# Kernel tuning notes

Hardware: AMD Instinct MI355X
Metric: run time of the kernel (lower is better)

## Reference

```python
import jax, jax.numpy as jnp
from jax import lax
import numpy as np

N_FFT = 256
HOP = 128
NUM_EXPERTS = 8
TOPK = 2
B = 128
L = 4096


def conv1d(x, w, b, pad):
    # x [N,C,T], w [O,I,K]
    y = lax.conv_general_dilated(x, w, (1,), [(pad, pad)],
                                 dimension_numbers=('NCH', 'OIH', 'NCH'))
    return y + b[None, :, None]


def maxpool1d(x, p):
    return lax.reduce_window(x, -jnp.inf, lax.max, (1, 1, p), (1, 1, p), 'VALID')


def se_block(x, w1, w2):
    # x [B,C,T]; squeeze-excitation with no-bias linears
    y = x.mean(-1)
    y = jax.nn.relu(y @ w1.T)
    y = jax.nn.sigmoid(y @ w2.T)
    return x * y[:, :, None]


def interp_linear(x, out_len):
    # F.interpolate(mode='linear', align_corners=False) on [B,C,T]
    Lin = x.shape[-1]
    scale = Lin / out_len
    coords = jnp.clip((jnp.arange(out_len, dtype=x.dtype) + 0.5) * scale - 0.5, 0.0, Lin - 1)
    lo = jnp.floor(coords).astype(jnp.int32)
    hi = jnp.minimum(lo + 1, Lin - 1)
    w = (coords - lo).astype(x.dtype)
    return x[..., lo] * (1.0 - w) + x[..., hi] * w


def lstm_scan(x, wih, whh, bih, bhh):
    # x [T,B,D] -> hidden seq [T,B,H]; torch gate order i,f,g,o
    H = whh.shape[1]
    def step(carry, xt):
        h, c = carry
        gates = xt @ wih.T + h @ whh.T + bih + bhh
        i, f, g, o = jnp.split(gates, 4, axis=-1)
        c = jax.nn.sigmoid(f) * c + jax.nn.sigmoid(i) * jnp.tanh(g)
        h = jax.nn.sigmoid(o) * jnp.tanh(c)
        return (h, c), h
    z = jnp.zeros((x.shape[1], H), x.dtype)
    _, hs = lax.scan(step, (z, z), x)
    return hs


def _forward(x_continuum, x_normalized,
             gate_w1, gate_b1, gate_w2, gate_b2,
             exp_w1, exp_b1, exp_w2, exp_b2,
             lw1, lb1, lw2, lb2, se2_w1, se2_w2, lw3, lb3, se3_w1, se3_w2,
             wih_f, whh_f, bih_f, bhh_f, wih_b, whh_b, bih_b, bhh_b,
             ffn_w1, ffn_b1, ffn_w2, ffn_b2):
    Bsz = x_continuum.shape[0]
    # --- STFT magnitude (center=True, reflect pad, periodic hann window) ---
    n = jnp.arange(N_FFT, dtype=x_continuum.dtype)
    win = 0.5 * (1.0 - jnp.cos(2.0 * jnp.pi * n / N_FFT))
    xp = jnp.pad(x_continuum, ((0, 0), (N_FFT // 2, N_FFT // 2)), mode='reflect')
    n_frames = 1 + (xp.shape[1] - N_FFT) // HOP  # 33
    idx = jnp.arange(n_frames)[:, None] * HOP + jnp.arange(N_FFT)[None, :]
    frames = xp[:, idx] * win                      # [B,T,N_FFT]
    mag = jnp.abs(jnp.fft.rfft(frames, axis=-1)).transpose(0, 2, 1)  # [B,129,T]
    mag = mag.astype(x_continuum.dtype)
    # --- gating: mean-pool over time, MLP, top-k, softmax over top-k ---
    pooled = mag.mean(-1)                          # [B,129]
    logits = jax.nn.relu(pooled @ gate_w1.T + gate_b1) @ gate_w2.T + gate_b2
    topv, topi = lax.top_k(logits, TOPK)
    gw = jax.nn.softmax(topv, axis=1)              # [B,K]
    # --- dense all-expert conv pyramids (matches original dense compute) ---
    def expert(w1, b1, w2, b2):
        h = jax.nn.relu(conv1d(mag, w1, b1, 2))
        return jax.nn.relu(conv1d(h, w2, b2, 1))
    eo = jax.vmap(expert)(exp_w1, exp_b1, exp_w2, exp_b2)  # [E,B,C,T]
    sel = eo[topi, jnp.arange(Bsz)[:, None]]               # [B,K,C,T]
    freq_feat = jnp.einsum('bk,bkct->bct', gw, sel)        # [B,256,33]
    # --- line attention branch ---
    h = jax.nn.relu(conv1d(x_normalized[:, None, :], lw1, lb1, 3))
    h = maxpool1d(h, 4)
    h = jax.nn.relu(conv1d(h, lw2, lb2, 2))
    h = se_block(h, se2_w1, se2_w2)
    h = maxpool1d(h, 4)
    h = jax.nn.relu(conv1d(h, lw3, lb3, 1))
    h = se_block(h, se3_w1, se3_w2)
    line_feat = maxpool1d(h, 4)                            # [B,256,64]
    # --- length alignment via linear interpolation ---
    t = min(freq_feat.shape[-1], line_feat.shape[-1])
    freq_feat = interp_linear(freq_feat, t)
    line_feat = interp_linear(line_feat, t)
    comb = jnp.concatenate([freq_feat, line_feat], axis=1).transpose(2, 0, 1)  # [T,B,512]
    # --- single-layer bidirectional LSTM, take last time step ---
    hf = lstm_scan(comb, wih_f, whh_f, bih_f, bhh_f)
    hb = lstm_scan(comb[::-1], wih_b, whh_b, bih_b, bhh_b)[::-1]
    last = jnp.concatenate([hf[-1], hb[-1]], axis=-1)      # [B,512]
    # --- prediction head (dropout inactive at inference) ---
    h = jax.nn.relu(last @ ffn_w1.T + ffn_b1)
    return h @ ffn_w2.T + ffn_b2                           # [B,1]


def setup_inputs() -> dict:
    key = jax.random.key(0)
    ks = jax.random.split(key, 40)
    def rn(k, shape, s=0.05):
        return jax.random.normal(k, shape, dtype=jnp.float32) * s
    d = {
        'x_continuum': jax.random.normal(ks[0], (B, L), jnp.float32),
        'x_normalized': jax.random.normal(ks[1], (B, L), jnp.float32),
        'gate_w1': rn(ks[2], (128, 129)), 'gate_b1': rn(ks[3], (128,)),
        'gate_w2': rn(ks[4], (NUM_EXPERTS, 128)), 'gate_b2': rn(ks[5], (NUM_EXPERTS,)),
        'exp_w1': rn(ks[6], (NUM_EXPERTS, 256, 129, 5)), 'exp_b1': rn(ks[7], (NUM_EXPERTS, 256)),
        'exp_w2': rn(ks[8], (NUM_EXPERTS, 256, 256, 3)), 'exp_b2': rn(ks[9], (NUM_EXPERTS, 256)),
        'lw1': rn(ks[10], (64, 1, 7)), 'lb1': rn(ks[11], (64,)),
        'lw2': rn(ks[12], (128, 64, 5)), 'lb2': rn(ks[13], (128,)),
        'se2_w1': rn(ks[14], (32, 128)), 'se2_w2': rn(ks[15], (128, 32)),
        'lw3': rn(ks[16], (256, 128, 3)), 'lb3': rn(ks[17], (256,)),
        'se3_w1': rn(ks[18], (64, 256)), 'se3_w2': rn(ks[19], (256, 64)),
        'wih_f': rn(ks[20], (1024, 512)), 'whh_f': rn(ks[21], (1024, 256)),
        'bih_f': rn(ks[22], (1024,)), 'bhh_f': rn(ks[23], (1024,)),
        'wih_b': rn(ks[24], (1024, 512)), 'whh_b': rn(ks[25], (1024, 256)),
        'bih_b': rn(ks[26], (1024,)), 'bhh_b': rn(ks[27], (1024,)),
        'ffn_w1': rn(ks[28], (256, 512)), 'ffn_b1': rn(ks[29], (256,)),
        'ffn_w2': rn(ks[30], (1, 256)), 'ffn_b2': rn(ks[31], (1,)),
    }
    return d


def reference(x_continuum, x_normalized,
              gate_w1, gate_b1, gate_w2, gate_b2,
              exp_w1, exp_b1, exp_w2, exp_b2,
              lw1, lb1, lw2, lb2, se2_w1, se2_w2, lw3, lb3, se3_w1, se3_w2,
              wih_f, whh_f, bih_f, bhh_f, wih_b, whh_b, bih_b, bhh_b,
              ffn_w1, ffn_b1, ffn_w2, ffn_b2):
    return _forward(x_continuum, x_normalized,
                    gate_w1, gate_b1, gate_w2, gate_b2,
                    exp_w1, exp_b1, exp_w2, exp_b2,
                    lw1, lb1, lw2, lb2, se2_w1, se2_w2, lw3, lb3, se3_w1, se3_w2,
                    wih_f, whh_f, bih_f, bhh_f, wih_b, whh_b, bih_b, bhh_b,
                    ffn_w1, ffn_b1, ffn_w2, ffn_b2)
```

## Files before the change

### kernel.cpp

```cpp
#include <hip/hip_runtime.h>
#include <math.h>

namespace {
constexpr int B = 128;
constexpr int L = 4096;
constexpr int NBIN = 129;
constexpr int NFR = 33;

constexpr size_t F_MAG    = 0;
constexpr size_t F_GW     = F_MAG + 544896;
constexpr size_t F_TOPI   = F_GW + 256;
constexpr size_t F_EH1    = F_TOPI + 256;
constexpr size_t F_SEL    = F_EH1 + 2162688;
constexpr size_t F_LINEF  = F_SEL + 2162688;
constexpr size_t F_COMB   = F_LINEF + 2097152;
constexpr size_t F_XPROJ  = F_COMB + 2162688;
constexpr size_t F_GATESB = F_XPROJ + 4325376;
constexpr size_t F_HF     = F_GATESB + 131072;
constexpr size_t F_HBLAST = F_HF + 32768;
constexpr size_t F_SESUM2 = F_HBLAST + 32768;
constexpr size_t F_SESC2  = F_SESUM2 + 16384;
constexpr size_t F_SESUM3 = F_SESC2 + 16384;
constexpr size_t F_SESC3  = F_SESUM3 + 32768;
constexpr size_t F_WHHB   = F_SESC3 + 32768;
constexpr size_t F_WKB    = F_WHHB + 131072;
constexpr size_t F_WKB3   = F_WKB + 20480;
constexpr size_t F_WIHF   = F_WKB3 + 49152;
constexpr size_t F_WIHB   = F_WIHF + 262144;
constexpr size_t F_BIGA   = F_WIHB + 262144;
constexpr size_t F_BIGB   = F_BIGA + 8388608;
constexpr size_t A_WKBE1  = F_XPROJ;
constexpr size_t A_WKBE2  = F_XPROJ + 720896;
constexpr size_t A_MAGT   = F_XPROJ + 1507328;

constexpr int PB_E1   = 5632;
constexpr int PB_E2   = PB_E1 + 6144;
constexpr int PB_WKB  = PB_E2 + 160;
constexpr int PB_WKB3 = PB_WKB + 384;
constexpr int PB_WF   = PB_WKB3 + 512;
constexpr int PB_WB   = PB_WF + 512;
constexpr int PB_WHH  = PB_WB + 128;
constexpr int PB_Z2   = PB_WHH + 64;
constexpr int PB_Z3   = PB_Z2 + 128;
}

typedef __attribute__((ext_vector_type(8))) short bf16x8;
typedef __attribute__((ext_vector_type(4))) float f32x4;

__device__ __forceinline__ float sigm(float x) { return 1.0f / (1.0f + expf(-x)); }
__device__ __forceinline__ float fsigm(float x) { return 1.0f / (1.0f + __expf(-x)); }
__device__ __forceinline__ float ftanh(float x) { return 1.0f - 2.0f / (__expf(2.0f * x) + 1.0f); }

__device__ __forceinline__ unsigned int f2bf_rne(float f) {
    unsigned int u = __float_as_uint(f);
    return (u + 0x7FFFu + ((u >> 16) & 1u)) >> 16;
}
__device__ __forceinline__ float bflo(unsigned int u) { return __uint_as_float(u << 16); }
__device__ __forceinline__ float bfhi(unsigned int u) { return __uint_as_float(u & 0xFFFF0000u); }
__device__ __forceinline__ float bf2f(unsigned short s) { return __uint_as_float(((unsigned int)s) << 16); }

__global__ __launch_bounds__(256) void prep_all_kernel(const float* __restrict__ exp_w1,
                                                       const float* __restrict__ exp_w2,
                                                       const float* __restrict__ lw2,
                                                       const float* __restrict__ lw3,
                                                       const float* __restrict__ wih_f,
                                                       const float* __restrict__ wih_b,
                                                       const float* __restrict__ whh_f,
                                                       unsigned short* __restrict__ wkbE1,
                                                       unsigned short* __restrict__ wkbE2,
                                                       unsigned short* __restrict__ wkb,
                                                       unsigned short* __restrict__ wkb3,
                                                       unsigned short* __restrict__ wihFb,
                                                       unsigned short* __restrict__ wihBb,
                                                       uint4* __restrict__ whh4,
                                                       float* __restrict__ seSum2,
                                                       float* __restrict__ seSum3)
{
    int bid = blockIdx.x, tid = threadIdx.x;
    if (bid < PB_E1) {
        int idx = bid * 256 + tid;
        int eo = idx / 704, K = idx % 704;
        int k = K / 136, ic = K - k * 136;
        float v = (k < 5 && ic < 129) ? exp_w1[((size_t)eo * 129 + ic) * 5 + k] : 0.f;
        wkbE1[idx] = (unsigned short)f2bf_rne(v);
    } else if (bid < PB_E2) {
        int idx = (bid - PB_E1) * 256 + tid;
        int eo = idx / 768, K = idx % 768;
        int k = K >> 8, ic = K & 255;
        wkbE2[idx] = (unsigned short)f2bf_rne(exp_w2[((size_t)eo * 256 + ic) * 3 + k]);
    } else if (bid < PB_WKB) {
        int idx = (bid - PB_E2) * 256 + tid;
        int oc = idx / 320, K = idx % 320;
        int k = K >> 6, ic = K & 63;
        wkb[idx] = (unsigned short)f2bf_rne(lw2[oc * 320 + ic * 5 + k]);
    } else if (bid < PB_WKB3) {
        int idx = (bid - PB_WKB) * 256 + tid;
        int oc = idx / 384, K = idx % 384;
        int k = K >> 7, ic = K & 127;
        wkb3[idx] = (unsigned short)f2bf_rne(lw3[oc * 384 + ic * 3 + k]);
    } else if (bid < PB_WF) {
        int i = ((bid - PB_WKB3) * 256 + tid) * 4;
        float4 v = *reinterpret_cast<const float4*>(wih_f + i);
        uint2 w;
        w.x = f2bf_rne(v.x) | (f2bf_rne(v.y) << 16);
        w.y = f2bf_rne(v.z) | (f2bf_rne(v.w) << 16);
        *reinterpret_cast<uint2*>(wihFb + i) = w;
    } else if (bid < PB_WB) {
        int i = ((bid - PB_WF) * 256 + tid) * 4;
        float4 v = *reinterpret_cast<const float4*>(wih_b + i);
        uint2 w;
        w.x = f2bf_rne(v.x) | (f2bf_rne(v.y) << 16);
        w.y = f2bf_rne(v.z) | (f2bf_rne(v.w) << 16);
        *reinterpret_cast<uint2*>(wihBb + i) = w;
    } else if (bid < PB_WHH) {
        int idx = (bid - PB_WB) * 256 + tid;
        int k8 = idx >> 10, j = idx & 1023;
        const float* src = whh_f + (size_t)j * 256 + k8 * 8;
        float4 v0 = *reinterpret_cast<const float4*>(src);
        float4 v1 = *reinterpret_cast<const float4*>(src + 4);
        uint4 w;
        w.x = f2bf_rne(v0.x) | (f2bf_rne(v0.y) << 16);
        w.y = f2bf_rne(v0.z) | (f2bf_rne(v0.w) << 16);
        w.z = f2bf_rne(v1.x) | (f2bf_rne(v1.y) << 16);
        w.w = f2bf_rne(v1.z) | (f2bf_rne(v1.w) << 16);
        whh4[(size_t)k8 * 1024 + j] = w;
    } else if (bid < PB_Z2) {
        seSum2[(bid - PB_WHH) * 256 + tid] = 0.f;
    } else {
        seSum3[(bid - PB_Z2) * 256 + tid] = 0.f;
    }
}

__global__ __launch_bounds__(256) void stft_kernel(const float* __restrict__ x,
                                                   float* __restrict__ mag,
                                                   unsigned short* __restrict__ magT)
{
    int bf = blockIdx.x;
    int b = bf / NFR, f = bf % NFR;
    int tid = threadIdx.x;
    __shared__ float tbl[256];
    __shared__ float fx[256];
    tbl[tid] = cosf(6.28318530717958647692f * (float)tid / 256.0f);
    __syncthreads();
    {
        int j = f * 128 + tid - 128;
        if (j < 0) j = -j;
        else if (j >= L) j = 2 * L - 2 - j;
        float win = 0.5f * (1.0f - tbl[tid]);
        fx[tid] = x[(size_t)b * L + j] * win;
    }
    __syncthreads();
    if (tid < NBIN) {
        float re = 0.f, im = 0.f;
        int m = 0;
        for (int n = 0; n < 256; ++n) {
            float v = fx[n];
            re += v * tbl[m];
            im += v * tbl[(m + 192) & 255];
            m = (m + tid) & 255;
        }
        float val = sqrtf(re * re + im * im);
        mag[((size_t)b * NBIN + tid) * NFR + f] = val;
        magT[((size_t)b * NFR + f) * 136 + tid] = (unsigned short)f2bf_rne(val);
    } else if (tid < 136) {
        magT[((size_t)b * NFR + f) * 136 + tid] = 0;
    }
}

__global__ __launch_bounds__(128) void gate_kernel(const float* __restrict__ mag,
                                                   const float* __restrict__ w1,
                                                   const float* __restrict__ b1,
                                                   const float* __restrict__ w2,
                                                   const float* __restrict__ b2,
                                                   int* __restrict__ topi,
                                                   float* __restrict__ gw)
{
    int b = blockIdx.x, tid = threadIdx.x;
    __shared__ float pooled[NBIN];
    __shared__ float h1[128];
    __shared__ float lg[8];
    for (int k = tid; k < NBIN; k += 128) {
        const float* mp = mag + ((size_t)b * NBIN + k) * NFR;
        float s = 0.f;
        for (int f = 0; f < NFR; ++f) s += mp[f];
        pooled[k] = s * (1.0f / 33.0f);
    }
    __syncthreads();
    {
        float acc = b1[tid];
        const float* wr = w1 + tid * NBIN;
        for (int k = 0; k < NBIN; ++k) acc += pooled[k] * wr[k];
        h1[tid] = fmaxf(acc, 0.f);
    }
    __syncthreads();
    if (tid < 8) {
        float a = b2[tid];
        const float* w = w2 + tid * 128;
        for (int j = 0; j < 128; ++j) a += h1[j] * w[j];
        lg[tid] = a;
    }
    __syncthreads();
    if (tid == 0) {
        int i0 = 0; float v0 = lg[0];
        for (int e = 1; e < 8; ++e) if (lg[e] > v0) { v0 = lg[e]; i0 = e; }
        int i1 = -1; float v1 = -3.0e38f;
        for (int e = 0; e < 8; ++e) { if (e == i0) continue; if (lg[e] > v1) { v1 = lg[e]; i1 = e; } }
        float m = fmaxf(v0, v1);
        float e0 = expf(v0 - m), e1 = expf(v1 - m);
        float inv = 1.0f / (e0 + e1);
        topi[b * 2 + 0] = i0; topi[b * 2 + 1] = i1;
        gw[b * 2 + 0] = e0 * inv; gw[b * 2 + 1] = e1 * inv;
    }
}

__global__ __launch_bounds__(256) void expert_conv1_mfma(const unsigned short* __restrict__ magT,
                                                         const int* __restrict__ topi,
                                                         const unsigned short* __restrict__ wkbE1,
                                                         const float* __restrict__ Bb,
                                                         unsigned short* __restrict__ eh1T)
{
    int b = blockIdx.x, slot = blockIdx.y, ocq = blockIdx.z;
    int e = topi[b * 2 + slot];
    __shared__ __align__(16) unsigned short wl[64 * 704];
    __shared__ __align__(16) unsigned short inT[37 * 136];
    __shared__ float bias[64];
    int tid = threadIdx.x;
    for (int idx = tid; idx < 64 * 88; idx += 256) {
        int oc = idx / 88, ch = idx % 88;
        int swz = (ch & ~7) | ((ch & 7) ^ (oc & 7));
        *reinterpret_cast<uint4*>(&wl[oc * 704 + swz * 8]) =
            *reinterpret_cast<const uint4*>(&wkbE1[((size_t)(e * 256 + ocq * 64 + oc)) * 704 + ch * 8]);
    }
    for (int idx = tid; idx < 37 * 17; idx += 256) {
        int j = idx / 17, ch = idx % 17;
        int tp = j - 2;
        uint4 v = make_uint4(0u, 0u, 0u, 0u);
        if (tp >= 0 && tp < 33)
            v = *reinterpret_cast<const uint4*>(&magT[((size_t)b * NFR + tp) * 136 + ch * 8]);
        *reinterpret_cast<uint4*>(&inT[j * 136 + ch * 8]) = v;
    }
    if (tid < 64) bias[tid] = Bb[e * 256 + ocq * 64 + tid];
    __syncthreads();

    int lane = tid & 63, w = tid >> 6, l15 = lane & 15, g = lane >> 4;
    f32x4 acc[3];
#pragma unroll
    for (int n = 0; n < 3; ++n) acc[n] = (f32x4){0.f, 0.f, 0.f, 0.f};

    int row = w * 16 + l15;
    for (int ks = 0; ks < 22; ++ks) {
        int ch = ks * 4 + g;
        bf16x8 af = *reinterpret_cast<const bf16x8*>(
            &wl[row * 704 + (((ch & ~7) | ((ch & 7) ^ (row & 7)))) * 8]);
        int ce = ch > 84 ? 84 : ch;
        int k = ce / 17, icc = ce - k * 17;
#pragma unroll
        for (int n = 0; n < 3; ++n) {
            int t = n * 16 + l15;
            int j = t + k; if (j > 36) j = 36;
            bf16x8 bf = *reinterpret_cast<const bf16x8*>(&inT[j * 136 + icc * 8]);
            acc[n] = __builtin_amdgcn_mfma_f32_16x16x32_bf16(af, bf, acc[n], 0, 0, 0);
        }
    }
#pragma unroll
    for (int n = 0; n < 3; ++n) {
        int t = n * 16 + l15;
        if (t < 33) {
            float v0 = fmaxf(acc[n][0] + bias[w * 16 + g * 4 + 0], 0.f);
            float v1 = fmaxf(acc[n][1] + bias[w * 16 + g * 4 + 1], 0.f);
            float v2 = fmaxf(acc[n][2] + bias[w * 16 + g * 4 + 2], 0.f);
            float v3 = fmaxf(acc[n][3] + bias[w * 16 + g * 4 + 3], 0.f);
            uint2 pk;
            pk.x = f2bf_rne(v0) | (f2bf_rne(v1) << 16);
            pk.y = f2bf_rne(v2) | (f2bf_rne(v3) << 16);
            *reinterpret_cast<uint2*>(
                &eh1T[(((size_t)(b * 2 + slot)) * NFR + t) * 256 + ocq * 64 + w * 16 + g * 4]) = pk;
        }
    }
}

__global__ __launch_bounds__(256) void expert_conv2_mfma(const unsigned short* __restrict__ eh1T,
                                                         const int* __restrict__ topi,
                                                         const unsigned short* __restrict__ wkbE2,
                                                         const float* __restrict__ Bb,
                                                         float* __restrict__ sel)
{
    int b = blockIdx.x, slot = blockIdx.y, ocq = blockIdx.z;
    int e = topi[b * 2 + slot];
    __shared__ __align__(16) unsigned short wl[64 * 768];
    __shared__ __align__(16) unsigned short inT[35 * 256];
    __shared__ float bias[64];
    int tid = threadIdx.x;
    for (int idx = tid; idx < 64 * 96; idx += 256) {
        int oc = idx / 96, ch = idx % 96;
        int swz = (ch & ~7) | ((ch & 7) ^ (oc & 7));
        *reinterpret_cast<uint4*>(&wl[oc * 768 + swz * 8]) =
            *reinterpret_cast<const uint4*>(&wkbE2[((size_t)(e * 256 + ocq * 64 + oc)) * 768 + ch * 8]);
    }
    for (int idx = tid; idx < 35 * 32; idx += 256) {
        int j = idx / 32, ch = idx % 32;
        int tp = j - 1;
        uint4 v = make_uint4(0u, 0u, 0u, 0u);
        if (tp >= 0 && tp < 33)
            v = *reinterpret_cast<const uint4*>(&eh1T[(((size_t)(b * 2 + slot)) * NFR + tp) * 256 + ch * 8]);
        int swz = (ch & ~15) | ((ch & 15) ^ (j & 15));
        *reinterpret_cast<uint4*>(&inT[j * 256 + swz * 8]) = v;
    }
    if (tid < 64) bias[tid] = Bb[e * 256 + ocq * 64 + tid];
    __syncthreads();

    int lane = tid & 63, w = tid >> 6, l15 = lane & 15, g = lane >> 4;
    f32x4 acc[3];
#pragma unroll
    for (int n = 0; n < 3; ++n) acc[n] = (f32x4){0.f, 0.f, 0.f, 0.f};

    int row = w * 16 + l15;
    for (int ks = 0; ks < 24; ++ks) {
        int ch = ks * 4 + g;
        bf16x8 af = *reinterpret_cast<const bf16x8*>(
            &wl[row * 768 + (((ch & ~7) | ((ch & 7) ^ (row & 7)))) * 8]);
        int k = ch >> 5, icc = ch & 31;
#pragma unroll
        for (int n = 0; n < 3; ++n) {
            int t = n * 16 + l15;
            int j = t + k; if (j > 34) j = 34;
            int sz = (icc & ~15) | ((icc & 15) ^ (j & 15));
            bf16x8 bf = *reinterpret_cast<const bf16x8*>(&inT[j * 256 + sz * 8]);
            acc[n] = __builtin_amdgcn_mfma_f32_16x16x32_bf16(af, bf, acc[n], 0, 0, 0);
        }
    }
#pragma unroll
    for (int n = 0; n < 3; ++n) {
        int t = n * 16 + l15;
        if (t < 33) {
#pragma unroll
            for (int r = 0; r < 4; ++r) {
                int oc = ocq * 64 + w * 16 + g * 4 + r;
                float v = fmaxf(acc[n][r] + bias[w * 16 + g * 4 + r], 0.f);
                sel[(((size_t)b * 2 + slot) * 256 + oc) * NFR + t] = v;
            }
        }
    }
}

__global__ __launch_bounds__(256) void line1_kernel(const float* __restrict__ x,
                                                    const float* __restrict__ lw1,
                                                    const float* __restrict__ lb1,
                                                    unsigned short* __restrict__ p1T)
{
    int b = blockIdx.x;
    int P0 = blockIdx.y * 256;
    __shared__ float sx[1032];
    __shared__ float w[448];
    __shared__ float bb[64];
    __shared__ unsigned short sT[256 * 65];
    int tid = threadIdx.x;
    for (int i = tid; i < 448; i += 256) w[i] = lw1[i];
    for (int i = tid; i < 64; i += 256) bb[i] = lb1[i];
    int base = 4 * P0 - 3;
    for (int i = tid; i < 1032; i += 256) {
        int g = base + i;
        sx[i] = (g >= 0 && g < L) ? x[(size_t)b * L + g] : 0.f;
    }
    __syncthreads();
    int p = tid;
    for (int oc = 0; oc < 64; ++oc) {
        const float* wr = w + oc * 7;
        float best = -3.0e38f;
#pragma unroll
        for (int q = 0; q < 4; ++q) {
            const float* s = sx + 4 * p + q;
            float v = wr[0]*s[0] + wr[1]*s[1] + wr[2]*s[2] + wr[3]*s[3] + wr[4]*s[4] + wr[5]*s[5] + wr[6]*s[6];
            best = fmaxf(best, v);
        }
        float v = fmaxf(best + bb[oc], 0.f);
        sT[p * 65 + oc] = (unsigned short)f2bf_rne(v);
    }
    __syncthreads();
    unsigned int* outw = reinterpret_cast<unsigned int*>(p1T);
    for (int i2 = tid; i2 < 256 * 32; i2 += 256) {
        int row = i2 >> 5, dw = i2 & 31;
        unsigned int lo = sT[row * 65 + dw * 2];
        unsigned int hi = sT[row * 65 + dw * 2 + 1];
        outw[((size_t)b * 1024 + P0 + row) * 32 + dw] = lo | (hi << 16);
    }
}

__global__ __launch_bounds__(256) void line2_mfma_kernel(const unsigned short* __restrict__ p1T,
                                                         const unsigned short* __restrict__ wkb,
                                                         const float* __restrict__ lb2,
                                                         unsigned short* __restrict__ h2b,
                                                         float* __restrict__ seSum2)
{
    int b = blockIdx.x;
    int t0 = blockIdx.y * 128;
    __shared__ __align__(16) unsigned short wl[128 * 320];
    __shared__ __align__(16) unsigned short inT[132 * 64];
    __shared__ float bias[128];
    int tid = threadIdx.x;

    for (int idx = tid; idx < 128 * 40; idx += 256) {
        int oc = idx / 40, ch = idx % 40;
        int swz = (ch & ~7) | ((ch & 7) ^ (oc & 7));
        *reinterpret_cast<uint4*>(&wl[oc * 320 + swz * 8]) =
            *reinterpret_cast<const uint4*>(&wkb[oc * 320 + ch * 8]);
    }
    for (int idx = tid; idx < 132 * 8; idx += 256) {
        int j = idx / 8, ch = idx % 8;
        int t = t0 - 2 + j;
        uint4 v = make_uint4(0u, 0u, 0u, 0u);
        if (t >= 0 && t < 1024)
            v = *reinterpret_cast<const uint4*>(&p1T[((size_t)b * 1024 + t) * 64 + ch * 8]);
        int swz = ch ^ (j & 7);
        *reinterpret_cast<uint4*>(&inT[j * 64 + swz * 8]) = v;
    }
    if (tid < 128) bias[tid] = lb2[tid];
    __syncthreads();

    int lane = tid & 63;
    int w = tid >> 6;
    int l15 = lane & 15, g = lane >> 4;

    f32x4 acc[8][2];
#pragma unroll
    for (int ot = 0; ot < 8; ++ot) {
        acc[ot][0] = (f32x4){0.f, 0.f, 0.f, 0.f};
        acc[ot][1] = (f32x4){0.f, 0.f, 0.f, 0.f};
    }

    for (int ks = 0; ks < 10; ++ks) {
        int k = ks >> 1;
        bf16x8 bf0, bf1;
        {
            int j = w * 32 + l15 + k;
            int ch = (ks & 1) * 4 + g;
            bf0 = *reinterpret_cast<const bf16x8*>(&inT[j * 64 + (ch ^ (j & 7)) * 8]);
            int j1 = j + 16;
            bf1 = *reinterpret_cast<const bf16x8*>(&inT[j1 * 64 + (ch ^ (j1 & 7)) * 8]);
        }
#pragma unroll
        for (int ot = 0; ot < 8; ++ot) {
            int row = ot * 16 + l15;
            int ch = ks * 4 + g;
            int swz = (ch & ~7) | ((ch & 7) ^ (row & 7));
            bf16x8 af = *reinterpret_cast<const bf16x8*>(&wl[row * 320 + swz * 8]);
            acc[ot][0] = __builtin_amdgcn_mfma_f32_16x16x32_bf16(af, bf0, acc[ot][0], 0, 0, 0);
            acc[ot][1] = __builtin_amdgcn_mfma_f32_16x16x32_bf16(af, bf1, acc[ot][1], 0, 0, 0);
        }
    }

    int tcol = t0 + w * 32 + l15;
#pragma unroll
    for (int ot = 0; ot < 8; ++ot) {
#pragma unroll
        for (int r = 0; r < 4; ++r) {
            int oc = ot * 16 + g * 4 + r;
            float bv = bias[oc];
            float v0 = fmaxf(acc[ot][0][r] + bv, 0.f);
            float v1 = fmaxf(acc[ot][1][r] + bv, 0.f);
            unsigned short* hp = h2b + ((size_t)b * 128 + oc) * 1024 + tcol;
            hp[0] = (unsigned short)f2bf_rne(v0);
            hp[16] = (unsigned short)f2bf_rne(v1);
            float s = v0 + v1;
            s += __shfl_xor(s, 1);
            s += __shfl_xor(s, 2);
            s += __shfl_xor(s, 4);
            s += __shfl_xor(s, 8);
            if (l15 == 0) atomicAdd(&seSum2[b * 128 + oc], s);
        }
    }
}

__global__ __launch_bounds__(256) void pool2t_kernel(const unsigned short* __restrict__ h2b,
                                                     const float* __restrict__ seSum2,
                                                     const float* __restrict__ w1,
                                                     const float* __restrict__ w2,
                                                     unsigned short* __restrict__ p2T)
{
    int b = blockIdx.x, p = threadIdx.x;
    __shared__ float y[128];
    __shared__ float z[32];
    __shared__ float scale[128];
    __shared__ unsigned short sT[256 * 129];
    if (p < 128) y[p] = seSum2[b * 128 + p] * (1.0f / 1024.0f);
    __syncthreads();
    if (p < 32) {
        float a = 0.f;
        const float* wr = w1 + p * 128;
        for (int c = 0; c < 128; ++c) a += y[c] * wr[c];
        z[p] = fmaxf(a, 0.f);
    }
    __syncthreads();
    if (p < 128) {
        float a = 0.f;
        const float* wr = w2 + p * 32;
        for (int j = 0; j < 32; ++j) a += z[j] * wr[j];
        scale[p] = sigm(a);
    }
    __syncthreads();
    for (int c = 0; c < 128; ++c) {
        uint2 v = *reinterpret_cast<const uint2*>(&h2b[((size_t)b * 128 + c) * 1024 + 4 * p]);
        float m = fmaxf(fmaxf(bflo(v.x), bfhi(v.x)), fmaxf(bflo(v.y), bfhi(v.y))) * scale[c];
        sT[p * 129 + c] = (unsigned short)f2bf_rne(m);
    }
    __syncthreads();
    unsigned int* out = reinterpret_cast<unsigned int*>(p2T);
    for (int idx = p; idx < 256 * 64; idx += 256) {
        int row = idx >> 6, dw = idx & 63;
        unsigned int lo = sT[row * 129 + dw * 2];
        unsigned int hi = sT[row * 129 + dw * 2 + 1];
        out[((size_t)b * 256 + row) * 64 + dw] = lo | (hi << 16);
    }
}

__global__ __launch_bounds__(256) void line3_mfma_kernel(const unsigned short* __restrict__ p2T,
                                                         const unsigned short* __restrict__ wkb3,
                                                         const float* __restrict__ lb3,
                                                         unsigned short* __restrict__ h3b,
                                                         float* __restrict__ seSum3)
{
    int b = blockIdx.x;
    int oc0 = blockIdx.y * 128;
    int t0 = blockIdx.z * 128;
    __shared__ __align__(16) unsigned short wl[128 * 384];
    __shared__ __align__(16) unsigned short inT[130 * 128];
    __shared__ float bias[128];
    int tid = threadIdx.x;

    for (int idx = tid; idx < 128 * 48; idx += 256) {
        int oc = idx / 48, ch = idx % 48;
        int swz = (ch & ~7) | ((ch & 7) ^ (oc & 7));
        *reinterpret_cast<uint4*>(&wl[oc * 384 + swz * 8]) =
            *reinterpret_cast<const uint4*>(&wkb3[(size_t)(oc0 + oc) * 384 + ch * 8]);
    }
    for (int idx = tid; idx < 130 * 16; idx += 256) {
        int j = idx / 16, ch = idx % 16;
        int t = t0 - 1 + j;
        uint4 v = make_uint4(0u, 0u, 0u, 0u);
        if (t >= 0 && t < 256)
            v = *reinterpret_cast<const uint4*>(&p2T[((size_t)b * 256 + t) * 128 + ch * 8]);
        int swz = ch ^ (j & 15);
        *reinterpret_cast<uint4*>(&inT[j * 128 + swz * 8]) = v;
    }
    if (tid < 128) bias[tid] = lb3[oc0 + tid];
    __syncthreads();

    int lane = tid & 63;
    int w = tid >> 6;
    int l15 = lane & 15, g = lane >> 4;

    f32x4 acc[8][2];
#pragma unroll
    for (int ot = 0; ot < 8; ++ot) {
        acc[ot][0] = (f32x4){0.f, 0.f, 0.f, 0.f};
        acc[ot][1] = (f32x4){0.f, 0.f, 0.f, 0.f};
    }

    for (int ks = 0; ks < 12; ++ks) {
        int k = ks >> 2;
        int ch = (ks & 3) * 4 + g;
        bf16x8 bf0, bf1;
        {
            int j = w * 32 + l15 + k;
            bf0 = *reinterpret_cast<const bf16x8*>(&inT[j * 128 + (ch ^ (j & 15)) * 8]);
            int j1 = j + 16;
            bf1 = *reinterpret_cast<const bf16x8*>(&inT[j1 * 128 + (ch ^ (j1 & 15)) * 8]);
        }
#pragma unroll
        for (int ot = 0; ot < 8; ++ot) {
            int row = ot * 16 + l15;
            int wch = ks * 4 + g;
            int swz = (wch & ~7) | ((wch & 7) ^ (row & 7));
            bf16x8 af = *reinterpret_cast<const bf16x8*>(&wl[row * 384 + swz * 8]);
            acc[ot][0] = __builtin_amdgcn_mfma_f32_16x16x32_bf16(af, bf0, acc[ot][0], 0, 0, 0);
            acc[ot][1] = __builtin_amdgcn_mfma_f32_16x16x32_bf16(af, bf1, acc[ot][1], 0, 0, 0);
        }
    }

    int tcol = t0 + w * 32 + l15;
#pragma unroll
    for (int ot = 0; ot < 8; ++ot) {
#pragma unroll
        for (int r = 0; r < 4; ++r) {
            int ocl = ot * 16 + g * 4 + r;
            int oc = oc0 + ocl;
            float bv = bias[ocl];
            float v0 = fmaxf(acc[ot][0][r] + bv, 0.f);
            float v1 = fmaxf(acc[ot][1][r] + bv, 0.f);
            unsigned short* hp = h3b + ((size_t)b * 256 + oc) * 256 + tcol;
            hp[0] = (unsigned short)f2bf_rne(v0);
            hp[16] = (unsigned short)f2bf_rne(v1);
            float s = v0 + v1;
            s += __shfl_xor(s, 1);
            s += __shfl_xor(s, 2);
            s += __shfl_xor(s, 4);
            s += __shfl_xor(s, 8);
            if (l15 == 0) atomicAdd(&seSum3[b * 256 + oc], s);
        }
    }
}

__global__ __launch_bounds__(256) void pool3_kernel(const unsigned short* __restrict__ h3b,
                                                    const float* __restrict__ seSum3,
                                                    const float* __restrict__ w1,
                                                    const float* __restrict__ w2,
                                                    float* __restrict__ lineFeat)
{
    int b = blockIdx.x, tid = threadIdx.x;
    __shared__ float y[256];
    __shared__ float z[64];
    __shared__ float scale[256];
    y[tid] = seSum3[b * 256 + tid] * (1.0f / 256.0f);
    __syncthreads();
    if (tid < 64) {
        float a = 0.f;
        const float* wr = w1 + tid * 256;
        for (int c = 0; c < 256; ++c) a += y[c] * wr[c];
        z[tid] = fmaxf(a, 0.f);
    }
    __syncthreads();
    {
        float a = 0.f;
        const float* wr = w2 + tid * 64;
        for (int j = 0; j < 64; ++j) a += z[j] * wr[j];
        scale[tid] = sigm(a);
    }
    __syncthreads();
    for (int idx = tid; idx < 256 * 64; idx += 256) {
        int c = idx >> 6, p = idx & 63;
        uint2 v = *reinterpret_cast<const uint2*>(&h3b[(((size_t)b * 256 + c) * 256) + 4 * p]);
        float m = fmaxf(fmaxf(bflo(v.x), bfhi(v.x)), fmaxf(bflo(v.y), bfhi(v.y)));
        lineFeat[((size_t)b * 256 + c) * 64 + p] = m * scale[c];
    }
}

__global__ __launch_bounds__(256) void comb_kernel(const float* __restrict__ sel,
                                                   const float* __restrict__ gw,
                                                   const float* __restrict__ lineFeat,
                                                   unsigned short* __restrict__ combB)
{
    const int total = 33 * 128 * 512;
    for (int idx = blockIdx.x * 256 + threadIdx.x; idx < total; idx += gridDim.x * 256) {
        int c = idx & 511;
        int r = idx >> 9;
        int b = r & 127;
        int t = r >> 7;
        float v;
        if (c < 256) {
            float g0 = gw[b * 2 + 0], g1 = gw[b * 2 + 1];
            v = g0 * sel[(((size_t)b * 2 + 0) * 256 + c) * NFR + t]
              + g1 * sel[(((size_t)b * 2 + 1) * 256 + c) * NFR + t];
        } else {
            int cc = c - 256;
            float xc = ((float)t + 0.5f) * (64.0f / 33.0f) - 0.5f;
            xc = fminf(fmaxf(xc, 0.0f), 63.0f);
            int lo = (int)floorf(xc);
            int hi = lo + 1; if (hi > 63) hi = 63;
            float w = xc - (float)lo;
            const float* lp = lineFeat + ((size_t)b * 256 + cc) * 64;
            v = lp[lo] * (1.0f - w) + lp[hi] * w;
        }
        combB[idx] = (unsigned short)f2bf_rne(v);
    }
}

__global__ __launch_bounds__(256) void gemm_mfma_kernel(const unsigned short* __restrict__ A,
                                                        const unsigned short* __restrict__ W,
                                                        const float* __restrict__ b1,
                                                        const float* __restrict__ b2,
                                                        float* __restrict__ out)
{
    int row0 = blockIdx.x * 128;
    int col0 = blockIdx.y * 128;
    __shared__ __align__(16) unsigned short As[128 * 64];
    __shared__ __align__(16) unsigned short Bs[128 * 64];
    __shared__ float bias[128];
    int tid = threadIdx.x;
    if (tid < 128) bias[tid] = b1[col0 + tid] + b2[col0 + tid];
    int lane = tid & 63, w = tid >> 6, l15 = lane & 15, g = lane >> 4;

    f32x4 acc[8][2];
#pragma unroll
    for (int ot = 0; ot < 8; ++ot) {
        acc[ot][0] = (f32x4){0.f, 0.f, 0.f, 0.f};
        acc[ot][1] = (f32x4){0.f, 0.f, 0.f, 0.f};
    }

    for (int kc = 0; kc < 8; ++kc) {
        __syncthreads();
        for (int idx = tid; idx < 1024; idx += 256) {
            int r = idx >> 3, ch = idx & 7;
            int swz = ch ^ (r & 7);
            *reinterpret_cast<uint4*>(&As[r * 64 + swz * 8]) =
                *reinterpret_cast<const uint4*>(&A[(size_t)(row0 + r) * 512 + kc * 64 + ch * 8]);
            *reinterpret_cast<uint4*>(&Bs[r * 64 + swz * 8]) =
                *reinterpret_cast<const uint4*>(&W[(size_t)(col0 + r) * 512 + kc * 64 + ch * 8]);
        }
        __syncthreads();
#pragma unroll
        for (int ks = 0; ks < 2; ++ks) {
            int ch = ks * 4 + g;
            int j = w * 32 + l15;
            bf16x8 bf0 = *reinterpret_cast<const bf16x8*>(&As[j * 64 + (ch ^ (j & 7)) * 8]);
            int j1 = j + 16;
            bf16x8 bf1 = *reinterpret_cast<const bf16x8*>(&As[j1 * 64 + (ch ^ (j1 & 7)) * 8]);
#pragma unroll
            for (int ot = 0; ot < 8; ++ot) {
                int row = ot * 16 + l15;
                bf16x8 af = *reinterpret_cast<const bf16x8*>(&Bs[row * 64 + (ch ^ (row & 7)) * 8]);
                acc[ot][0] = __builtin_amdgcn_mfma_f32_16x16x32_bf16(af, bf0, acc[ot][0], 0, 0, 0);
                acc[ot][1] = __builtin_amdgcn_mfma_f32_16x16x32_bf16(af, bf1, acc[ot][1], 0, 0, 0);
            }
        }
    }

    int rbase = row0 + w * 32 + l15;
#pragma unroll
    for (int ot = 0; ot < 8; ++ot) {
#pragma unroll
        for (int r = 0; r < 4; ++r) {
            int ocl = ot * 16 + g * 4 + r;
            float bv = bias[ocl];
            out[(size_t)rbase * 1024 + col0 + ocl] = acc[ot][0][r] + bv;
            out[(size_t)(rbase + 16) * 1024 + col0 + ocl] = acc[ot][1][r] + bv;
        }
    }
}

__global__ __launch_bounds__(1024) void lstm_fused_kernel(const float* __restrict__ xproj,
                                                          const uint4* __restrict__ whh4,
                                                          float* __restrict__ hfinal)
{
    int b = blockIdx.x;
    int j = threadIdx.x;
    __shared__ __align__(16) float h[256];
    __shared__ float cc[256];
    __shared__ float g[1024];
    if (j < 256) { h[j] = 0.f; cc[j] = 0.f; }
    __syncthreads();
    const uint4* wp = whh4 + j;
    for (int t = 0; t < 33; ++t) {
        float a0 = xproj[(size_t)t * 131072 + (size_t)b * 1024 + j];
        float a1 = 0.f;
#pragma unroll 8
        for (int k8 = 0; k8 < 32; ++k8) {
            uint4 w = wp[k8 << 10];
            float4 h0 = *reinterpret_cast<const float4*>(&h[k8 * 8]);
            float4 h1 = *reinterpret_cast<const float4*>(&h[k8 * 8 + 4]);
            a0 += bflo(w.x) * h0.x + bfhi(w.x) * h0.y + bflo(w.y) * h0.z + bfhi(w.y) * h0.w;
            a1 += bflo(w.z) * h1.x + bfhi(w.z) * h1.y + bflo(w.w) * h1.z + bfhi(w.w) * h1.w;
        }
        g[j] = a0 + a1;
        __syncthreads();
        if (j < 256) {
            float gi = g[j], gf = g[256 + j], gz = g[512 + j], go = g[768 + j];
            float c = fsigm(gf) * cc[j] + fsigm(gi) * ftanh(gz);
            cc[j] = c;
            h[j] = fsigm(go) * ftanh(c);
        }
        __syncthreads();
    }
    if (j < 256) hfinal[b * 256 + j] = h[j];
}

__global__ __launch_bounds__(256) void ffn_kernel(const float* __restrict__ hf,
                                                  const float* __restrict__ gatesB,
                                                  const float* __restrict__ w1,
                                                  const float* __restrict__ b1,
                                                  const float* __restrict__ w2,
                                                  const float* __restrict__ b2,
                                                  float* __restrict__ out)
{
    int b = blockIdx.x, tid = threadIdx.x;
    __shared__ float last[512];
    __shared__ float red[256];
    last[tid] = hf[b * 256 + tid];
    {
        const float* g = gatesB + (size_t)b * 1024;
        float ai = g[tid], ag = g[512 + tid], ao = g[768 + tid];
        float c = sigm(ai) * tanhf(ag);
        last[256 + tid] = sigm(ao) * tanhf(c);
    }
    __syncthreads();
    float a = b1[tid];
    const float* wr = w1 + (size_t)tid * 512;
    for (int k = 0; k < 512; ++k) a += last[k] * wr[k];
    red[tid] = fmaxf(a, 0.f) * w2[tid];
    __syncthreads();
    for (int s = 128; s > 0; s >>= 1) {
        if (tid < s) red[tid] += red[tid + s];
        __syncthreads();
    }
    if (tid == 0) out[b] = red[0] + b2[0];
}

extern "C" void kernel_launch(void* const* d_in, const int* in_sizes, int n_in,
                              void* d_out, int out_size, void* d_ws, size_t ws_size,
                              hipStream_t stream)
{
    (void)in_sizes; (void)n_in; (void)out_size; (void)ws_size;
    const float* x_cont = (const float*)d_in[0];
    const float* x_norm = (const float*)d_in[1];
    const float* gate_w1 = (const float*)d_in[2];
    const float* gate_b1 = (const float*)d_in[3];
    const float* gate_w2 = (const float*)d_in[4];
    const float* gate_b2 = (const float*)d_in[5];
    const float* exp_w1 = (const float*)d_in[6];
    const float* exp_b1 = (const float*)d_in[7];
    const float* exp_w2 = (const float*)d_in[8];
    const float* exp_b2 = (const float*)d_in[9];
    const float* lw1 = (const float*)d_in[10];
    const float* lb1 = (const float*)d_in[11];
    const float* lw2 = (const float*)d_in[12];
    const float* lb2 = (const float*)d_in[13];
    const float* se2_w1 = (const float*)d_in[14];
    const float* se2_w2 = (const float*)d_in[15];
    const float* lw3 = (const float*)d_in[16];
    const float* lb3 = (const float*)d_in[17];
    const float* se3_w1 = (const float*)d_in[18];
    const float* se3_w2 = (const float*)d_in[19];
    const float* wih_f = (const float*)d_in[20];
    const float* whh_f = (const float*)d_in[21];
    const float* bih_f = (const float*)d_in[22];
    const float* bhh_f = (const float*)d_in[23];
    const float* wih_b = (const float*)d_in[24];
    const float* whh_b = (const float*)d_in[25];
    const float* bih_b = (const float*)d_in[26];
    const float* bhh_b = (const float*)d_in[27];
    const float* ffn_w1 = (const float*)d_in[28];
    const float* ffn_b1 = (const float*)d_in[29];
    const float* ffn_w2 = (const float*)d_in[30];
    const float* ffn_b2 = (const float*)d_in[31];

    float* ws = (float*)d_ws;
    float* mag     = ws + F_MAG;
    float* gw      = ws + F_GW;
    int*   topi    = (int*)(ws + F_TOPI);
    unsigned short* eh1T = (unsigned short*)(ws + F_EH1);
    float* sel     = ws + F_SEL;
    float* lineFeat= ws + F_LINEF;
    unsigned short* combB = (unsigned short*)(ws + F_COMB);
    float* xproj   = ws + F_XPROJ;
    float* gatesB  = ws + F_GATESB;
    float* hfF     = ws + F_HF;
    float* seSum2  = ws + F_SESUM2;
    float* seSum3  = ws + F_SESUM3;
    uint4* whh4    = (uint4*)(ws + F_WHHB);
    unsigned short* wkb  = (unsigned short*)(ws + F_WKB);
    unsigned short* wkb3 = (unsigned short*)(ws + F_WKB3);
    unsigned short* wihFb = (unsigned short*)(ws + F_WIHF);
    unsigned short* wihBb = (unsigned short*)(ws + F_WIHB);
    unsigned short* wkbE1 = (unsigned short*)(ws + A_WKBE1);
    unsigned short* wkbE2 = (unsigned short*)(ws + A_WKBE2);
    unsigned short* magT  = (unsigned short*)(ws + A_MAGT);
    unsigned short* p1T = (unsigned short*)(ws + F_BIGA);
    unsigned short* h2b = (unsigned short*)(ws + F_BIGB);
    unsigned short* p2T = (unsigned short*)(ws + F_BIGA);
    unsigned short* h3b = (unsigned short*)(ws + F_BIGB);

    prep_all_kernel<<<PB_Z3, 256, 0, stream>>>(exp_w1, exp_w2, lw2, lw3, wih_f, wih_b, whh_f,
                                               wkbE1, wkbE2, wkb, wkb3, wihFb, wihBb, whh4,
                                               seSum2, seSum3);

    stft_kernel<<<B * NFR, 256, 0, stream>>>(x_cont, mag, magT);
    gate_kernel<<<B, 128, 0, stream>>>(mag, gate_w1, gate_b1, gate_w2, gate_b2, topi, gw);
    expert_conv1_mfma<<<dim3(B, 2, 4), 256, 0, stream>>>(magT, topi, wkbE1, exp_b1, eh1T);
    expert_conv2_mfma<<<dim3(B, 2, 4), 256, 0, stream>>>(eh1T, topi, wkbE2, exp_b2, sel);

    line1_kernel<<<dim3(B, 4), 256, 0, stream>>>(x_norm, lw1, lb1, p1T);
    line2_mfma_kernel<<<dim3(B, 8), 256, 0, stream>>>(p1T, wkb, lb2, h2b, seSum2);
    pool2t_kernel<<<B, 256, 0, stream>>>(h2b, seSum2, se2_w1, se2_w2, p2T);
    line3_mfma_kernel<<<dim3(B, 2, 2), 256, 0, stream>>>(p2T, wkb3, lb3, h3b, seSum3);
    pool3_kernel<<<B, 256, 0, stream>>>(h3b, seSum3, se3_w1, se3_w2, lineFeat);

    comb_kernel<<<2048, 256, 0, stream>>>(sel, gw, lineFeat, combB);

    gemm_mfma_kernel<<<dim3(33, 8), 256, 0, stream>>>(combB, wihFb, bih_f, bhh_f, xproj);
    gemm_mfma_kernel<<<dim3(1, 8), 256, 0, stream>>>(combB + (size_t)4096 * 512, wihBb, bih_b, bhh_b, gatesB);

    lstm_fused_kernel<<<B, 1024, 0, stream>>>(xproj, whh4, hfF);

    ffn_kernel<<<B, 256, 0, stream>>>(hfF, gatesB, ffn_w1, ffn_b1, ffn_w2, ffn_b2, (float*)d_out);
}
```

Baseline: 562.4 us.

## Fuse pool3 into comb kernel with transposed expert output layout

```diff
diff --git a/kernel.cpp b/kernel.cpp
--- a/kernel.cpp
+++ b/kernel.cpp
@@ -57,7 +57,6 @@
 }
 __device__ __forceinline__ float bflo(unsigned int u) { return __uint_as_float(u << 16); }
 __device__ __forceinline__ float bfhi(unsigned int u) { return __uint_as_float(u & 0xFFFF0000u); }
-__device__ __forceinline__ float bf2f(unsigned short s) { return __uint_as_float(((unsigned int)s) << 16); }
 
 __global__ __launch_bounds__(256) void prep_all_kernel(const float* __restrict__ exp_w1,
                                                        const float* __restrict__ exp_w2,
@@ -283,7 +282,7 @@
                                                          const int* __restrict__ topi,
                                                          const unsigned short* __restrict__ wkbE2,
                                                          const float* __restrict__ Bb,
-                                                         float* __restrict__ sel)
+                                                         float* __restrict__ selT)
 {
     int b = blockIdx.x, slot = blockIdx.y, ocq = blockIdx.z;
     int e = topi[b * 2 + slot];
@@ -337,7 +336,7 @@
             for (int r = 0; r < 4; ++r) {
                 int oc = ocq * 64 + w * 16 + g * 4 + r;
                 float v = fmaxf(acc[n][r] + bias[w * 16 + g * 4 + r], 0.f);
-                sel[(((size_t)b * 2 + slot) * 256 + oc) * NFR + t] = v;
+                selT[(((size_t)(b * 2 + slot)) * NFR + t) * 256 + oc] = v;
             }
         }
     }
@@ -600,16 +599,19 @@
     }
 }
 
-__global__ __launch_bounds__(256) void pool3_kernel(const unsigned short* __restrict__ h3b,
-                                                    const float* __restrict__ seSum3,
-                                                    const float* __restrict__ w1,
-                                                    const float* __restrict__ w2,
-                                                    float* __restrict__ lineFeat)
+__global__ __launch_bounds__(256) void comb_pool3_kernel(const unsigned short* __restrict__ h3b,
+                                                         const float* __restrict__ seSum3,
+                                                         const float* __restrict__ w1,
+                                                         const float* __restrict__ w2,
+                                                         const float* __restrict__ selT,
+                                                         const float* __restrict__ gw,
+                                                         unsigned short* __restrict__ combB)
 {
     int b = blockIdx.x, tid = threadIdx.x;
     __shared__ float y[256];
     __shared__ float z[64];
     __shared__ float scale[256];
+    __shared__ float lf[256 * 64];
     y[tid] = seSum3[b * 256 + tid] * (1.0f / 256.0f);
     __syncthreads();
     if (tid < 64) {
@@ -630,26 +632,18 @@
         int c = idx >> 6, p = idx & 63;
         uint2 v = *reinterpret_cast<const uint2*>(&h3b[(((size_t)b * 256 + c) * 256) + 4 * p]);
         float m = fmaxf(fmaxf(bflo(v.x), bfhi(v.x)), fmaxf(bflo(v.y), bfhi(v.y)));
-        lineFeat[((size_t)b * 256 + c) * 64 + p] = m * scale[c];
-    }
-}
-
-__global__ __launch_bounds__(256) void comb_kernel(const float* __restrict__ sel,
-                                                   const float* __restrict__ gw,
-                                                   const float* __restrict__ lineFeat,
-                                                   unsigned short* __restrict__ combB)
-{
-    const int total = 33 * 128 * 512;
-    for (int idx = blockIdx.x * 256 + threadIdx.x; idx < total; idx += gridDim.x * 256) {
+        lf[c * 64 + p] = m * scale[c];
+    }
+    __syncthreads();
+    float g0 = gw[b * 2 + 0], g1 = gw[b * 2 + 1];
+    const float* s0 = selT + ((size_t)(b * 2 + 0)) * NFR * 256;
+    const float* s1 = selT + ((size_t)(b * 2 + 1)) * NFR * 256;
+    for (int idx = tid; idx < NFR * 512; idx += 256) {
         int c = idx & 511;
-        int r = idx >> 9;
-        int b = r & 127;
-        int t = r >> 7;
+        int t = idx >> 9;
         float v;
         if (c < 256) {
-            float g0 = gw[b * 2 + 0], g1 = gw[b * 2 + 1];
-            v = g0 * sel[(((size_t)b * 2 + 0) * 256 + c) * NFR + t]
-              + g1 * sel[(((size_t)b * 2 + 1) * 256 + c) * NFR + t];
+            v = g0 * s0[t * 256 + c] + g1 * s1[t * 256 + c];
         } else {
             int cc = c - 256;
             float xc = ((float)t + 0.5f) * (64.0f / 33.0f) - 0.5f;
@@ -657,10 +651,10 @@
             int lo = (int)floorf(xc);
             int hi = lo + 1; if (hi > 63) hi = 63;
             float w = xc - (float)lo;
-            const float* lp = lineFeat + ((size_t)b * 256 + cc) * 64;
+            const float* lp = lf + cc * 64;
             v = lp[lo] * (1.0f - w) + lp[hi] * w;
         }
-        combB[idx] = (unsigned short)f2bf_rne(v);
+        combB[((size_t)t * 128 + b) * 512 + c] = (unsigned short)f2bf_rne(v);
     }
 }
 
@@ -772,7 +766,7 @@
                                                   float* __restrict__ out)
 {
     int b = blockIdx.x, tid = threadIdx.x;
-    __shared__ float last[512];
+    __shared__ __align__(16) float last[512];
     __shared__ float red[256];
     last[tid] = hf[b * 256 + tid];
     {
@@ -783,8 +777,13 @@
     }
     __syncthreads();
     float a = b1[tid];
-    const float* wr = w1 + (size_t)tid * 512;
-    for (int k = 0; k < 512; ++k) a += last[k] * wr[k];
+    const float4* wr4 = reinterpret_cast<const float4*>(w1 + (size_t)tid * 512);
+    const float4* l4 = reinterpret_cast<const float4*>(last);
+    for (int k = 0; k < 128; ++k) {
+        float4 wv = wr4[k];
+        float4 lv = l4[k];
+        a += wv.x * lv.x + wv.y * lv.y + wv.z * lv.z + wv.w * lv.w;
+    }
     red[tid] = fmaxf(a, 0.f) * w2[tid];
     __syncthreads();
     for (int s = 128; s > 0; s >>= 1) {
@@ -837,8 +836,7 @@
     float* gw      = ws + F_GW;
     int*   topi    = (int*)(ws + F_TOPI);
     unsigned short* eh1T = (unsigned short*)(ws + F_EH1);
-    float* sel     = ws + F_SEL;
-    float* lineFeat= ws + F_LINEF;
+    float* selT    = ws + F_SEL;
     unsigned short* combB = (unsigned short*)(ws + F_COMB);
     float* xproj   = ws + F_XPROJ;
     float* gatesB  = ws + F_GATESB;
@@ -865,15 +863,14 @@
     stft_kernel<<<B * NFR, 256, 0, stream>>>(x_cont, mag, magT);
     gate_kernel<<<B, 128, 0, stream>>>(mag, gate_w1, gate_b1, gate_w2, gate_b2, topi, gw);
     expert_conv1_mfma<<<dim3(B, 2, 4), 256, 0, stream>>>(magT, topi, wkbE1, exp_b1, eh1T);
-    expert_conv2_mfma<<<dim3(B, 2, 4), 256, 0, stream>>>(eh1T, topi, wkbE2, exp_b2, sel);
+    expert_conv2_mfma<<<dim3(B, 2, 4), 256, 0, stream>>>(eh1T, topi, wkbE2, exp_b2, selT);
 
     line1_kernel<<<dim3(B, 4), 256, 0, stream>>>(x_norm, lw1, lb1, p1T);
     line2_mfma_kernel<<<dim3(B, 8), 256, 0, stream>>>(p1T, wkb, lb2, h2b, seSum2);
     pool2t_kernel<<<B, 256, 0, stream>>>(h2b, seSum2, se2_w1, se2_w2, p2T);
     line3_mfma_kernel<<<dim3(B, 2, 2), 256, 0, stream>>>(p2T, wkb3, lb3, h3b, seSum3);
-    pool3_kernel<<<B, 256, 0, stream>>>(h3b, seSum3, se3_w1, se3_w2, lineFeat);
-
-    comb_kernel<<<2048, 256, 0, stream>>>(sel, gw, lineFeat, combB);
+
+    comb_pool3_kernel<<<B, 256, 0, stream>>>(h3b, seSum3, se3_w1, se3_w2, selT, gw, combB);
 
     gemm_mfma_kernel<<<dim3(33, 8), 256, 0, stream>>>(combB, wihFb, bih_f, bhh_f, xproj);
     gemm_mfma_kernel<<<dim3(1, 8), 256, 0, stream>>>(combB + (size_t)4096 * 512, wihBb, bih_b, bhh_b, gatesB);
```

Result: no change. 563.7 us (+0.2%).
